# Optimization experiments

Hardware: AMD Instinct MI355X
Metric: run time of the kernel (lower is better)

## Reference

```python
import jax, jax.numpy as jnp
import numpy as np
import math

STATE_DIM = 512
NUM_GROUPS = 32
VMD_MODES = 8
PERM_DIM = 4
MAX_PATTERNS = math.factorial(PERM_DIM)  # 24


def setup_inputs() -> dict:
    key = jax.random.key(0)
    B, T = 16, 4096
    hidden_states = jax.random.normal(key, (B, T, STATE_DIM), dtype=jnp.float32)
    return {"hidden_states": hidden_states}


def _vmd_decomposition(signals):
    # signals: [B, G, T] -> modes [B, G, K, T]
    B, G, T = signals.shape
    K = VMD_MODES
    fft_signal = jnp.fft.fft(signals, axis=2)
    freqs = jnp.fft.fftfreq(T).astype(jnp.float32)
    bandwidth = 1.0 / K
    center_freqs = jnp.linspace(-0.5, 0.5, K, dtype=jnp.float32)
    dist = jnp.abs(freqs[None, :] - center_freqs[:, None])          # [K, T]
    filters = jnp.exp(-0.5 * (dist / bandwidth) ** 2)
    filtered = fft_signal[:, :, None, :] * filters[None, None, :, :]
    return jnp.fft.ifft(filtered, axis=3).real.astype(jnp.float32)


def _pattern_ids(windows):
    # windows: [B, G, K, N, m] -> Lehmer-code pattern ids [B, G, K, N]
    m = windows.shape[-1]
    si = jnp.argsort(windows, axis=-1)
    fact = [math.factorial(j) for j in range(m)]
    pid = jnp.zeros(windows.shape[:-1], dtype=jnp.int32)
    for i in range(m - 1):
        smaller = (si[..., i:i + 1] > si[..., i + 1:]).sum(axis=-1).astype(jnp.int32)
        pid = pid + smaller * fact[m - 1 - i]
    return pid


def _tmptm(modes):
    # modes: [B, G, K, T] -> normalized transition histogram [B, G, MP^2]
    B, G, K, T = modes.shape
    m, MP = PERM_DIM, MAX_PATTERNS
    N = T - m + 1
    # unfold(3, m, 1): [B, G, K, N, m]
    windows = jnp.stack([modes[..., i:i + N] for i in range(m)], axis=-1)
    pid = _pattern_ids(windows)                       # [B, G, K, N]
    lin = pid[..., :-1] * MP + pid[..., 1:]           # [B, G, K, N-1]
    # fused scatter-add histogram over (K, N-1) per (B, G) -- replaces one_hot+sum
    offset = jnp.arange(B * G, dtype=jnp.int32).reshape(B, G, 1, 1) * (MP * MP)
    flat = (lin + offset).reshape(-1)
    counts = jnp.zeros(B * G * MP * MP, dtype=jnp.float32).at[flat].add(1.0)
    tmptm = counts.reshape(B, G, MP * MP)
    row_sums = jnp.maximum(tmptm.sum(axis=2, keepdims=True), 1.0)
    return tmptm / row_sums


def _fmptm(modes):
    # modes: [B, G, K, T] -> upper-triangular energy correlations [B, G, K*(K-1)/2]
    B, G, K, T = modes.shape
    energies = modes ** 2
    mean_e = energies.mean(axis=3, keepdims=True)
    std_e = jnp.maximum(energies.std(axis=3, keepdims=True, ddof=1), 1e-8)  # torch std is unbiased
    ne = (energies - mean_e) / std_e
    corr = jnp.einsum('bgkt,bglt->bgkl', ne, ne) / T
    iu, ju = jnp.triu_indices(K, k=1)
    return corr[:, :, iu, ju]


def reference(hidden_states):
    B, T, D = hidden_states.shape
    G = NUM_GROUPS
    spg = D // G
    hs = hidden_states.astype(jnp.float32)
    hs = hs.transpose(0, 2, 1).reshape(B, G, spg, T)
    group_pooled = hs.mean(axis=2)                    # [B, G, T]
    modes = _vmd_decomposition(group_pooled)          # [B, G, K, T]
    tmptm = _tmptm(modes)
    fmptm = _fmptm(modes)
    return tmptm, fmptm
```

## Files before the change

### kernel.cpp

```cpp
#include <hip/hip_runtime.h>
#include <hip/hip_fp16.h>

#define TT   4096
#define NTH  512
#define SK(e) ((e) + (((e) >> 4) << 1))
#define ARR  4608
#define SM_FLOATS (4*ARR + 1152 + 44)
#define SM_BYTES  (SM_FLOATS * 4)

__device__ __forceinline__ float centerF(int k){
    return (float)(-0.5 + (double)k * (1.0/7.0));
}
__device__ __forceinline__ float freq_of(int m){
    return (float)((m < TT/2) ? m : (m - TT)) * (1.0f/(float)TT);
}
__device__ __forceinline__ float filtv(float f, float ck){
    float d = (f - ck) * 8.0f;
    return __expf(-0.5f * d * d);
}
__device__ __forceinline__ float Gval(int m, float ck){
    int mm = (TT - m) & (TT - 1);
    return (filtv(freq_of(m), ck) + filtv(freq_of(mm), ck)) * (0.5f/(float)TT);
}

struct C4 { float r0,i0,r1,i1,r2,i2,r3,i3; };

template<int SGN>
__device__ __forceinline__ void bf4(float c0r,float c0i,float c1r,float c1i,
                                    float c2r,float c2i,float c3r,float c3i,
                                    float ur,float ui, C4& o){
    float u2r = ur*ur - ui*ui, u2i = 2.f*ur*ui;
    float u3r = u2r*ur - u2i*ui, u3i = u2r*ui + u2i*ur;
    if (SGN < 0){ ui = -ui; u2i = -u2i; u3i = -u3i; }
    float ar = u2r*c2r - u2i*c2i, ai = u2r*c2i + u2i*c2r;
    float br = ur*c1r  - ui*c1i,  bi = ur*c1i  + ui*c1r;
    float er = u3r*c3r - u3i*c3i, ei = u3r*c3i + u3i*c3r;
    float s0r = c0r+ar, s0i = c0i+ai, s1r = c0r-ar, s1i = c0i-ai;
    float s2r = br+er,  s2i = bi+ei,  s3r = br-er,  s3i = bi-ei;
    o.r0 = s0r+s2r; o.i0 = s0i+s2i;
    o.r2 = s0r-s2r; o.i2 = s0i-s2i;
    if (SGN > 0){ o.r1 = s1r-s3i; o.i1 = s1i+s3r; o.r3 = s1r+s3i; o.i3 = s1i-s3r; }
    else        { o.r1 = s1r+s3i; o.i1 = s1i-s3r; o.r3 = s1r-s3i; o.i3 = s1i+s3r; }
}

template<int SGN>
__device__ __forceinline__ void stageLDS(const float* __restrict__ sr, const float* __restrict__ si,
                                         float* __restrict__ dr, float* __restrict__ di,
                                         int Ns, float uAr,float uAi,float uBr,float uBi, int tid){
#pragma unroll
    for (int h = 0; h < 2; ++h){
        int j = tid + h*512;
        float ur = h ? uBr : uAr, ui = h ? uBi : uAi;
        int kk = j & (Ns-1);
        int base = ((j & ~(Ns-1)) << 2) | kk;
        C4 o;
        bf4<SGN>(sr[SK(j)],si[SK(j)], sr[SK(j+1024)],si[SK(j+1024)],
                 sr[SK(j+2048)],si[SK(j+2048)], sr[SK(j+3072)],si[SK(j+3072)], ur,ui,o);
        dr[SK(base)]       = o.r0;  di[SK(base)]       = o.i0;
        dr[SK(base+Ns)]    = o.r1;  di[SK(base+Ns)]    = o.i1;
        dr[SK(base+2*Ns)]  = o.r2;  di[SK(base+2*Ns)]  = o.i2;
        dr[SK(base+3*Ns)]  = o.r3;  di[SK(base+3*Ns)]  = o.i3;
    }
}

__device__ __forceinline__ int wt_of(int r){ return r==0 ? 6 : (r==1 ? 2 : (r==2 ? 1 : 0)); }

__device__ __forceinline__ int pattern_id(float v0, float v1, float v2, float v3){
    int c01 = (v0 <= v1), c02 = (v0 <= v2), c03 = (v0 <= v3);
    int c12 = (v1 <= v2), c13 = (v1 <= v3), c23 = (v2 <= v3);
    int r1 = c01 + (1-c12) + (1-c13);
    int r2 = c02 + c12 + (1-c23);
    int r3 = c03 + c13 + c23;
    int g1 = 1 - c01;
    int g2 = (1-c02) + (1-c12);
    int g3 = (1-c03) + (1-c13) + (1-c23);
    return wt_of(r1)*g1 + wt_of(r2)*g2 + wt_of(r3)*g3;
}

__device__ __forceinline__ int DIDX(int k, int l){
    return 8 + k*8 + l - (k*(k+1))/2;
}

__device__ __forceinline__ void reduce_to(float v, float* res, int idx, int tid){
#pragma unroll
    for (int off = 32; off; off >>= 1) v += __shfl_xor(v, off);
    if ((tid & 63) == 0) atomicAdd(&res[idx], v);
}

template<int P>
__device__ __forceinline__ void process_pair(int tid,
        float* Ar, float* Ai, float* Br, float* Bi,
        unsigned* hist, float* res,
        const float (&xr)[8], const float (&xi)[8],
        __half2 (&est)[6][4],
        float t4r,float t4i,float t16r,float t16i,float t64r,float t64i,
        float t256r,float t256i,float tAr,float tAi,float tBr,float tBi){
    const float ck0 = centerF(2*P), ck1 = centerF(2*P+1);

#pragma unroll
    for (int h = 0; h < 2; ++h){
        int j = tid + h*512;
        float cr[4], ci[4];
#pragma unroll
        for (int q = 0; q < 4; ++q){
            int v = 2*q + h;
            int m = j + 1024*q;
            float g0 = Gval(m, ck0), g1 = Gval(m, ck1);
            cr[q] = xr[v]*g0 - xi[v]*g1;
            ci[q] = xi[v]*g0 + xr[v]*g1;
        }
        C4 o; bf4<1>(cr[0],ci[0],cr[1],ci[1],cr[2],ci[2],cr[3],ci[3], 1.f,0.f, o);
        int base = 4*j;
        Ar[SK(base)]   = o.r0;  Ai[SK(base)]   = o.i0;
        Ar[SK(base+1)] = o.r1;  Ai[SK(base+1)] = o.i1;
        Ar[SK(base+2)] = o.r2;  Ai[SK(base+2)] = o.i2;
        Ar[SK(base+3)] = o.r3;  Ai[SK(base+3)] = o.i3;
    }
    __syncthreads();
    stageLDS<1>(Ar,Ai,Br,Bi,    4, t4r,t4i,t4r,t4i, tid);       __syncthreads();
    stageLDS<1>(Br,Bi,Ar,Ai,   16, t16r,t16i,t16r,t16i, tid);   __syncthreads();
    stageLDS<1>(Ar,Ai,Br,Bi,   64, t64r,t64i,t64r,t64i, tid);   __syncthreads();
    stageLDS<1>(Br,Bi,Ar,Ai,  256, t256r,t256i,t256r,t256i, tid); __syncthreads();
    stageLDS<1>(Ar,Ai,Br,Bi, 1024, tAr,tAi,tBr,tBi, tid);       __syncthreads();

    int* pidR = (int*)Ar;
    int* pidI = (int*)Ai;

    float aS0=0.f, aS1=0.f, aD00=0.f, aD11=0.f, aD01=0.f;
    float aX[(P > 0) ? 4*P : 1];
#pragma unroll
    for (int i = 0; i < ((P>0)?4*P:1); ++i) aX[i] = 0.f;

    float carry0 = 0.f, carry1 = 0.f;
#pragma unroll
    for (int u = 0; u < 8; ++u){
        int t  = tid + u*NTH;
        int t1 = (t+1 < TT) ? t+1 : TT-1;
        int t2 = (t+2 < TT) ? t+2 : TT-1;
        int t3 = (t+3 < TT) ? t+3 : TT-1;
        float b0 = Br[SK(t)], b1 = Br[SK(t1)], b2 = Br[SK(t2)], b3 = Br[SK(t3)];
        float i0 = Bi[SK(t)], i1 = Bi[SK(t1)], i2 = Bi[SK(t2)], i3 = Bi[SK(t3)];
        float e0 = b0*b0, e1 = i0*i0;
        aS0 += e0; aS1 += e1;
        aD00 += e0*e0; aD11 += e1*e1; aD01 += e0*e1;
#pragma unroll
        for (int l = 0; l < 2*P; ++l){
            float el = (u & 1) ? __high2float(est[l][u>>1]) : __low2float(est[l][u>>1]);
            aX[2*l]   += el * e0;
            aX[2*l+1] += el * e1;
        }
        if constexpr (P < 3){
            if ((u & 1) == 0){ carry0 = e0; carry1 = e1; }
            else {
                est[2*P][u>>1]   = __floats2half2_rn(carry0, e0);
                est[2*P+1][u>>1] = __floats2half2_rn(carry1, e1);
            }
        }
        if (t <= TT-4){
            pidR[t] = pattern_id(b0,b1,b2,b3);
            pidI[t] = pattern_id(i0,i1,i2,i3);
        }
    }
    __syncthreads();

    {
        unsigned* h = hist + 576*((tid>>6) & 1);
        int curR = -1, curI = -1; unsigned cR = 0, cI = 0;
#pragma unroll
        for (int u = 0; u < 8; ++u){
            int t = tid + u*NTH;
            if (t <= TT-5){
                int lr = pidR[t]*24 + pidR[t+1];
                if (lr == curR) cR++;
                else { if (cR) atomicAdd(&h[curR], cR); curR = lr; cR = 1; }
                int li = pidI[t]*24 + pidI[t+1];
                if (li == curI) cI++;
                else { if (cI) atomicAdd(&h[curI], cI); curI = li; cI = 1; }
            }
        }
        if (cR) atomicAdd(&h[curR], cR);
        if (cI) atomicAdd(&h[curI], cI);
    }
    __syncthreads();

    const int k0 = 2*P, k1 = 2*P+1;
    reduce_to(aS0,  res, k0, tid);
    reduce_to(aS1,  res, k1, tid);
    reduce_to(aD00, res, DIDX(k0,k0), tid);
    reduce_to(aD11, res, DIDX(k1,k1), tid);
    reduce_to(aD01, res, DIDX(k0,k1), tid);
#pragma unroll
    for (int l = 0; l < 2*P; ++l){
        reduce_to(aX[2*l],   res, DIDX(l,k0), tid);
        reduce_to(aX[2*l+1], res, DIDX(l,k1), tid);
    }
}

template<bool DIRECT>
__global__ __launch_bounds__(NTH)
__attribute__((amdgpu_waves_per_eu(4,4)))
void fused_kernel(const float* __restrict__ hs, const float* __restrict__ pooled,
                  float* __restrict__ out){
    extern __shared__ float smem[];
    float* Ar = smem;
    float* Ai = smem + ARR;
    float* Br = smem + 2*ARR;
    float* Bi = smem + 3*ARR;
    unsigned* hist = (unsigned*)(smem + 4*ARR);
    float* res = smem + 4*ARR + 1152;

    const int tid = threadIdx.x;
    const int bg = blockIdx.x, b = bg >> 5, g = bg & 31;

    for (int i = tid; i < 1152; i += NTH) hist[i] = 0u;
    if (tid < 44) res[tid] = 0.f;

    const float PI_F = 3.14159265358979323846f;
    float t4r,t4i,t16r,t16i,t64r,t64i,t256r,t256i,tAr,tAi,tBr,tBi;
    { float s,c;
      __sincosf(PI_F*(float)(tid &   3)/   8.f, &s,&c); t4r=c;   t4i=s;
      __sincosf(PI_F*(float)(tid &  15)/  32.f, &s,&c); t16r=c;  t16i=s;
      __sincosf(PI_F*(float)(tid &  63)/ 128.f, &s,&c); t64r=c;  t64i=s;
      __sincosf(PI_F*(float)(tid & 255)/ 512.f, &s,&c); t256r=c; t256i=s;
      __sincosf(PI_F*(float)tid        /2048.f, &s,&c); tAr=c;   tAi=s;
      __sincosf(PI_F*(float)(tid+512)  /2048.f, &s,&c); tBr=c;   tBi=s;
    }

    if (DIRECT){
        const float* base = hs + ((size_t)b * TT) * 512 + g * 16;
#pragma unroll
        for (int u = 0; u < 8; ++u){
            int t = tid + u*NTH;
            const float4* p = (const float4*)(base + (size_t)t * 512);
            float4 a = p[0], bb = p[1], cc = p[2], dd = p[3];
            float s = a.x+a.y+a.z+a.w + bb.x+bb.y+bb.z+bb.w
                    + cc.x+cc.y+cc.z+cc.w + dd.x+dd.y+dd.z+dd.w;
            Ar[SK(t)] = s * (1.0f/16.0f);
            Ai[SK(t)] = 0.f;
        }
    } else {
        const float* pp = pooled + (size_t)bg * TT;
#pragma unroll
        for (int u = 0; u < 8; ++u){
            int t = tid + u*NTH;
            Ar[SK(t)] = pp[t];
            Ai[SK(t)] = 0.f;
        }
    }
    __syncthreads();

    stageLDS<-1>(Ar,Ai,Br,Bi,   1, 1.f,0.f,1.f,0.f, tid);        __syncthreads();
    stageLDS<-1>(Br,Bi,Ar,Ai,   4, t4r,t4i,t4r,t4i, tid);        __syncthreads();
    stageLDS<-1>(Ar,Ai,Br,Bi,  16, t16r,t16i,t16r,t16i, tid);    __syncthreads();
    stageLDS<-1>(Br,Bi,Ar,Ai,  64, t64r,t64i,t64r,t64i, tid);    __syncthreads();
    stageLDS<-1>(Ar,Ai,Br,Bi, 256, t256r,t256i,t256r,t256i, tid);__syncthreads();

    float xr[8], xi[8];
    {
        C4 o;
        bf4<-1>(Br[SK(tid)],Bi[SK(tid)], Br[SK(tid+1024)],Bi[SK(tid+1024)],
                Br[SK(tid+2048)],Bi[SK(tid+2048)], Br[SK(tid+3072)],Bi[SK(tid+3072)],
                tAr,tAi,o);
        xr[0]=o.r0; xi[0]=o.i0; xr[2]=o.r1; xi[2]=o.i1;
        xr[4]=o.r2; xi[4]=o.i2; xr[6]=o.r3; xi[6]=o.i3;
        bf4<-1>(Br[SK(tid+512)],Bi[SK(tid+512)], Br[SK(tid+1536)],Bi[SK(tid+1536)],
                Br[SK(tid+2560)],Bi[SK(tid+2560)], Br[SK(tid+3584)],Bi[SK(tid+3584)],
                tBr,tBi,o);
        xr[1]=o.r0; xi[1]=o.i0; xr[3]=o.r1; xi[3]=o.i1;
        xr[5]=o.r2; xi[5]=o.i2; xr[7]=o.r3; xi[7]=o.i3;
    }

    __half2 est[6][4];
    process_pair<0>(tid,Ar,Ai,Br,Bi,hist,res,xr,xi,est,t4r,t4i,t16r,t16i,t64r,t64i,t256r,t256i,tAr,tAi,tBr,tBi);
    process_pair<1>(tid,Ar,Ai,Br,Bi,hist,res,xr,xi,est,t4r,t4i,t16r,t16i,t64r,t64i,t256r,t256i,tAr,tAi,tBr,tBi);
    process_pair<2>(tid,Ar,Ai,Br,Bi,hist,res,xr,xi,est,t4r,t4i,t16r,t16i,t64r,t64i,t256r,t256i,tAr,tAi,tBr,tBi);
    process_pair<3>(tid,Ar,Ai,Br,Bi,hist,res,xr,xi,est,t4r,t4i,t16r,t16i,t64r,t64i,t256r,t256i,tAr,tAi,tBr,tBi);

    __syncthreads();

    float* tm = out + (size_t)bg * 576;
    for (int i = tid; i < 576; i += NTH)
        tm[i] = (float)(hist[i] + hist[i+576]) * (1.0f/32736.0f);

    if (tid < 28){
        int q = tid, k = 0, cnt = 7, rem = q;
        while (rem >= cnt){ rem -= cnt; k++; cnt--; }
        int l = k + 1 + rem;
        float Sk = res[k], Sl = res[l];
        float Dkl = res[DIDX(k,l)], Dkk = res[DIDX(k,k)], Dll = res[DIDX(l,l)];
        float cov = Dkl - Sk*Sl*(1.0f/4096.0f);
        float vk = (Dkk - Sk*Sk*(1.0f/4096.0f)) * (1.0f/4095.0f);
        float vl = (Dll - Sl*Sl*(1.0f/4096.0f)) * (1.0f/4095.0f);
        float sk = fmaxf(sqrtf(fmaxf(vk, 0.f)), 1e-8f);
        float sl = fmaxf(sqrtf(fmaxf(vl, 0.f)), 1e-8f);
        out[294912 + (size_t)bg*28 + q] = cov * (1.0f/4096.0f) / (sk*sl);
    }
}

__global__ __launch_bounds__(256)
void pool_kernel(const float* __restrict__ hs, float* __restrict__ pooled){
    __shared__ float tile[32][65];
    int blk = blockIdx.x;
    int b   = blk >> 6;
    int t0  = (blk & 63) << 6;
    int tid = threadIdx.x;
    int lane = tid & 63, wid = tid >> 6;
#pragma unroll
    for (int i = 0; i < 16; ++i){
        int tl = wid + i*4;
        int t  = t0 + tl;
        const float4* p = (const float4*)(hs + ((size_t)b * TT + t) * 512);
        float4 a = p[lane];
        float4 c = p[lane + 64];
        float pa = a.x+a.y+a.z+a.w;
        float pc = c.x+c.y+c.z+c.w;
        pa += __shfl_xor(pa, 1); pa += __shfl_xor(pa, 2);
        pc += __shfl_xor(pc, 1); pc += __shfl_xor(pc, 2);
        if ((lane & 3) == 0){
            int gq = lane >> 2;
            tile[gq][tl]      = pa * (1.0f/16.0f);
            tile[gq + 16][tl] = pc * (1.0f/16.0f);
        }
    }
    __syncthreads();
    for (int idx = tid; idx < 2048; idx += 256){
        int g = idx >> 6, tt = idx & 63;
        pooled[((size_t)b * 32 + g) * TT + t0 + tt] = tile[g][tt];
    }
}

extern "C" void kernel_launch(void* const* d_in, const int* in_sizes, int n_in,
                              void* d_out, int out_size, void* d_ws, size_t ws_size,
                              hipStream_t stream){
    const float* hs = (const float*)d_in[0];
    float* out = (float*)d_out;
    const size_t poolBytes = (size_t)512 * TT * sizeof(float);

    if (d_ws && ws_size >= poolBytes){
        float* pooled = (float*)d_ws;
        pool_kernel<<<1024, 256, 0, stream>>>(hs, pooled);
        hipFuncSetAttribute((const void*)fused_kernel<false>,
                            hipFuncAttributeMaxDynamicSharedMemorySize, SM_BYTES);
        fused_kernel<false><<<512, NTH, SM_BYTES, stream>>>(hs, pooled, out);
    } else {
        hipFuncSetAttribute((const void*)fused_kernel<true>,
                            hipFuncAttributeMaxDynamicSharedMemorySize, SM_BYTES);
        fused_kernel<true><<<512, NTH, SM_BYTES, stream>>>(hs, nullptr, out);
    }
}
```

Measured before the change: 320.5 us.

## Switch 4096-point LDS FFT from radix-4 to radix-8 stages

```diff
diff --git a/kernel.cpp b/kernel.cpp
--- a/kernel.cpp
+++ b/kernel.cpp
@@ -3,8 +3,8 @@
 
 #define TT   4096
 #define NTH  512
-#define SK(e) ((e) + (((e) >> 4) << 1))
-#define ARR  4608
+#define SK(e) ((e) + ((e) >> 5))
+#define ARR  4224
 #define SM_FLOATS (4*ARR + 1152 + 44)
 #define SM_BYTES  (SM_FLOATS * 4)
 
@@ -23,43 +23,75 @@
     return (filtv(freq_of(m), ck) + filtv(freq_of(mm), ck)) * (0.5f/(float)TT);
 }
 
-struct C4 { float r0,i0,r1,i1,r2,i2,r3,i3; };
-
 template<int SGN>
-__device__ __forceinline__ void bf4(float c0r,float c0i,float c1r,float c1i,
-                                    float c2r,float c2i,float c3r,float c3i,
-                                    float ur,float ui, C4& o){
-    float u2r = ur*ur - ui*ui, u2i = 2.f*ur*ui;
-    float u3r = u2r*ur - u2i*ui, u3i = u2r*ui + u2i*ur;
-    if (SGN < 0){ ui = -ui; u2i = -u2i; u3i = -u3i; }
-    float ar = u2r*c2r - u2i*c2i, ai = u2r*c2i + u2i*c2r;
-    float br = ur*c1r  - ui*c1i,  bi = ur*c1i  + ui*c1r;
-    float er = u3r*c3r - u3i*c3i, ei = u3r*c3i + u3i*c3r;
-    float s0r = c0r+ar, s0i = c0i+ai, s1r = c0r-ar, s1i = c0i-ai;
-    float s2r = br+er,  s2i = bi+ei,  s3r = br-er,  s3i = bi-ei;
-    o.r0 = s0r+s2r; o.i0 = s0i+s2i;
-    o.r2 = s0r-s2r; o.i2 = s0i-s2i;
-    if (SGN > 0){ o.r1 = s1r-s3i; o.i1 = s1i+s3r; o.r3 = s1r+s3i; o.i3 = s1i-s3r; }
-    else        { o.r1 = s1r+s3i; o.i1 = s1i-s3r; o.r3 = s1r-s3i; o.i3 = s1i+s3r; }
-}
-
-template<int SGN>
-__device__ __forceinline__ void stageLDS(const float* __restrict__ sr, const float* __restrict__ si,
-                                         float* __restrict__ dr, float* __restrict__ di,
-                                         int Ns, float uAr,float uAi,float uBr,float uBi, int tid){
-#pragma unroll
-    for (int h = 0; h < 2; ++h){
-        int j = tid + h*512;
-        float ur = h ? uBr : uAr, ui = h ? uBi : uAi;
-        int kk = j & (Ns-1);
-        int base = ((j & ~(Ns-1)) << 2) | kk;
-        C4 o;
-        bf4<SGN>(sr[SK(j)],si[SK(j)], sr[SK(j+1024)],si[SK(j+1024)],
-                 sr[SK(j+2048)],si[SK(j+2048)], sr[SK(j+3072)],si[SK(j+3072)], ur,ui,o);
-        dr[SK(base)]       = o.r0;  di[SK(base)]       = o.i0;
-        dr[SK(base+Ns)]    = o.r1;  di[SK(base+Ns)]    = o.i1;
-        dr[SK(base+2*Ns)]  = o.r2;  di[SK(base+2*Ns)]  = o.i2;
-        dr[SK(base+3*Ns)]  = o.r3;  di[SK(base+3*Ns)]  = o.i3;
+__device__ __forceinline__ void bf8(float (&xr)[8], float (&xi)[8]){
+    const float C = 0.7071067811865476f;
+    float tr[4], ti[4], ur[4], ui[4];
+#pragma unroll
+    for (int p = 0; p < 4; ++p){
+        tr[p] = xr[p] + xr[p+4]; ti[p] = xi[p] + xi[p+4];
+        ur[p] = xr[p] - xr[p+4]; ui[p] = xi[p] - xi[p+4];
+    }
+    float vr[4], vi[4];
+    vr[0] = ur[0]; vi[0] = ui[0];
+    if (SGN > 0){
+        vr[1] =  C*(ur[1] - ui[1]); vi[1] =  C*(ur[1] + ui[1]);
+        vr[2] = -ui[2];             vi[2] =  ur[2];
+        vr[3] = -C*(ur[3] + ui[3]); vi[3] =  C*(ur[3] - ui[3]);
+    } else {
+        vr[1] =  C*(ur[1] + ui[1]); vi[1] =  C*(ui[1] - ur[1]);
+        vr[2] =  ui[2];             vi[2] = -ur[2];
+        vr[3] =  C*(ui[3] - ur[3]); vi[3] = -C*(ur[3] + ui[3]);
+    }
+    {
+        float s0r=tr[0]+tr[2], s0i=ti[0]+ti[2], s1r=tr[0]-tr[2], s1i=ti[0]-ti[2];
+        float s2r=tr[1]+tr[3], s2i=ti[1]+ti[3], s3r=tr[1]-tr[3], s3i=ti[1]-ti[3];
+        xr[0]=s0r+s2r; xi[0]=s0i+s2i;
+        xr[4]=s0r-s2r; xi[4]=s0i-s2i;
+        if (SGN > 0){ xr[2]=s1r-s3i; xi[2]=s1i+s3r; xr[6]=s1r+s3i; xi[6]=s1i-s3r; }
+        else        { xr[2]=s1r+s3i; xi[2]=s1i-s3r; xr[6]=s1r-s3i; xi[6]=s1i+s3r; }
+    }
+    {
+        float s0r=vr[0]+vr[2], s0i=vi[0]+vi[2], s1r=vr[0]-vr[2], s1i=vi[0]-vi[2];
+        float s2r=vr[1]+vr[3], s2i=vi[1]+vi[3], s3r=vr[1]-vr[3], s3i=vi[1]-vi[3];
+        xr[1]=s0r+s2r; xi[1]=s0i+s2i;
+        xr[5]=s0r-s2r; xi[5]=s0i-s2i;
+        if (SGN > 0){ xr[3]=s1r-s3i; xi[3]=s1i+s3r; xr[7]=s1r+s3i; xi[7]=s1i-s3r; }
+        else        { xr[3]=s1r+s3i; xi[3]=s1i-s3r; xr[7]=s1r-s3i; xi[7]=s1i+s3r; }
+    }
+}
+
+__device__ __forceinline__ void twid8(float (&xr)[8], float (&xi)[8], float wr, float wi){
+    float pr = wr, pi = wi;
+#pragma unroll
+    for (int q = 1; q < 8; ++q){
+        float ar = xr[q], ai = xi[q];
+        xr[q] = ar*pr - ai*pi;
+        xi[q] = ar*pi + ai*pr;
+        float nr = pr*wr - pi*wi;
+        float ni = pr*wi + pi*wr;
+        pr = nr; pi = ni;
+    }
+}
+
+template<int SGN, int NS>
+__device__ __forceinline__ void stage8(const float* __restrict__ sr, const float* __restrict__ si,
+                                       float* __restrict__ dr, float* __restrict__ di,
+                                       float wr, float wi, int tid){
+    float xr[8], xi[8];
+#pragma unroll
+    for (int q = 0; q < 8; ++q){
+        xr[q] = sr[SK(tid + 512*q)];
+        xi[q] = si[SK(tid + 512*q)];
+    }
+    if (NS > 1) twid8(xr, xi, wr, wi);
+    bf8<SGN>(xr, xi);
+    int kk = tid & (NS-1);
+    int base = ((tid & ~(NS-1)) << 3) | kk;
+#pragma unroll
+    for (int m = 0; m < 8; ++m){
+        dr[SK(base + m*NS)] = xr[m];
+        di[SK(base + m*NS)] = xi[m];
     }
 }
 
@@ -93,35 +125,45 @@
         unsigned* hist, float* res,
         const float (&xr)[8], const float (&xi)[8],
         __half2 (&est)[6][4],
-        float t4r,float t4i,float t16r,float t16i,float t64r,float t64i,
-        float t256r,float t256i,float tAr,float tAi,float tBr,float tBi){
+        float w8r,float w8i,float w64r,float w64i,float w512r,float w512i){
     const float ck0 = centerF(2*P), ck1 = centerF(2*P+1);
 
-#pragma unroll
-    for (int h = 0; h < 2; ++h){
-        int j = tid + h*512;
-        float cr[4], ci[4];
-#pragma unroll
-        for (int q = 0; q < 4; ++q){
-            int v = 2*q + h;
-            int m = j + 1024*q;
+    {
+        float cr[8], ci[8];
+#pragma unroll
+        for (int q = 0; q < 8; ++q){
+            int m = tid + 512*q;
             float g0 = Gval(m, ck0), g1 = Gval(m, ck1);
-            cr[q] = xr[v]*g0 - xi[v]*g1;
-            ci[q] = xi[v]*g0 + xr[v]*g1;
-        }
-        C4 o; bf4<1>(cr[0],ci[0],cr[1],ci[1],cr[2],ci[2],cr[3],ci[3], 1.f,0.f, o);
-        int base = 4*j;
-        Ar[SK(base)]   = o.r0;  Ai[SK(base)]   = o.i0;
-        Ar[SK(base+1)] = o.r1;  Ai[SK(base+1)] = o.i1;
-        Ar[SK(base+2)] = o.r2;  Ai[SK(base+2)] = o.i2;
-        Ar[SK(base+3)] = o.r3;  Ai[SK(base+3)] = o.i3;
-    }
-    __syncthreads();
-    stageLDS<1>(Ar,Ai,Br,Bi,    4, t4r,t4i,t4r,t4i, tid);       __syncthreads();
-    stageLDS<1>(Br,Bi,Ar,Ai,   16, t16r,t16i,t16r,t16i, tid);   __syncthreads();
-    stageLDS<1>(Ar,Ai,Br,Bi,   64, t64r,t64i,t64r,t64i, tid);   __syncthreads();
-    stageLDS<1>(Br,Bi,Ar,Ai,  256, t256r,t256i,t256r,t256i, tid); __syncthreads();
-    stageLDS<1>(Ar,Ai,Br,Bi, 1024, tAr,tAi,tBr,tBi, tid);       __syncthreads();
+            cr[q] = xr[q]*g0 - xi[q]*g1;
+            ci[q] = xi[q]*g0 + xr[q]*g1;
+        }
+        bf8<1>(cr, ci);
+        int base = 8*tid;
+#pragma unroll
+        for (int m = 0; m < 8; ++m){
+            Ar[SK(base+m)] = cr[m];
+            Ai[SK(base+m)] = ci[m];
+        }
+    }
+    __syncthreads();
+    stage8<1,8>(Ar,Ai,Br,Bi, w8r,w8i, tid);    __syncthreads();
+    stage8<1,64>(Br,Bi,Ar,Ai, w64r,w64i, tid); __syncthreads();
+
+    float yr[8], yi[8];
+#pragma unroll
+    for (int q = 0; q < 8; ++q){
+        yr[q] = Ar[SK(tid + 512*q)];
+        yi[q] = Ai[SK(tid + 512*q)];
+    }
+    twid8(yr, yi, w512r, w512i);
+    bf8<1>(yr, yi);
+#pragma unroll
+    for (int m = 0; m < 8; ++m){
+        int t = tid + 512*m;
+        Br[SK(t)] = yr[m];
+        Bi[SK(t)] = yi[m];
+    }
+    __syncthreads();
 
     int* pidR = (int*)Ar;
     int* pidI = (int*)Ai;
@@ -134,12 +176,13 @@
     float carry0 = 0.f, carry1 = 0.f;
 #pragma unroll
     for (int u = 0; u < 8; ++u){
-        int t  = tid + u*NTH;
+        int t  = tid + 512*u;
         int t1 = (t+1 < TT) ? t+1 : TT-1;
         int t2 = (t+2 < TT) ? t+2 : TT-1;
         int t3 = (t+3 < TT) ? t+3 : TT-1;
-        float b0 = Br[SK(t)], b1 = Br[SK(t1)], b2 = Br[SK(t2)], b3 = Br[SK(t3)];
-        float i0 = Bi[SK(t)], i1 = Bi[SK(t1)], i2 = Bi[SK(t2)], i3 = Bi[SK(t3)];
+        float b0 = yr[u],       i0 = yi[u];
+        float b1 = Br[SK(t1)],  b2 = Br[SK(t2)], b3 = Br[SK(t3)];
+        float j1 = Bi[SK(t1)],  j2 = Bi[SK(t2)], j3 = Bi[SK(t3)];
         float e0 = b0*b0, e1 = i0*i0;
         aS0 += e0; aS1 += e1;
         aD00 += e0*e0; aD11 += e1*e1; aD01 += e0*e1;
@@ -158,7 +201,7 @@
         }
         if (t <= TT-4){
             pidR[t] = pattern_id(b0,b1,b2,b3);
-            pidI[t] = pattern_id(i0,i1,i2,i3);
+            pidI[t] = pattern_id(i0,j1,j2,j3);
         }
     }
     __syncthreads();
@@ -168,7 +211,7 @@
         int curR = -1, curI = -1; unsigned cR = 0, cI = 0;
 #pragma unroll
         for (int u = 0; u < 8; ++u){
-            int t = tid + u*NTH;
+            int t = tid + 512*u;
             if (t <= TT-5){
                 int lr = pidR[t]*24 + pidR[t+1];
                 if (lr == curR) cR++;
@@ -181,7 +224,6 @@
         if (cR) atomicAdd(&h[curR], cR);
         if (cI) atomicAdd(&h[curI], cI);
     }
-    __syncthreads();
 
     const int k0 = 2*P, k1 = 2*P+1;
     reduce_to(aS0,  res, k0, tid);
@@ -194,11 +236,11 @@
         reduce_to(aX[2*l],   res, DIDX(l,k0), tid);
         reduce_to(aX[2*l+1], res, DIDX(l,k1), tid);
     }
+    __syncthreads();
 }
 
 template<bool DIRECT>
-__global__ __launch_bounds__(NTH)
-__attribute__((amdgpu_waves_per_eu(4,4)))
+__global__ __launch_bounds__(NTH, 1)
 void fused_kernel(const float* __restrict__ hs, const float* __restrict__ pooled,
                   float* __restrict__ out){
     extern __shared__ float smem[];
@@ -216,14 +258,11 @@
     if (tid < 44) res[tid] = 0.f;
 
     const float PI_F = 3.14159265358979323846f;
-    float t4r,t4i,t16r,t16i,t64r,t64i,t256r,t256i,tAr,tAi,tBr,tBi;
+    float w8r,w8i,w64r,w64i,w512r,w512i;
     { float s,c;
-      __sincosf(PI_F*(float)(tid &   3)/   8.f, &s,&c); t4r=c;   t4i=s;
-      __sincosf(PI_F*(float)(tid &  15)/  32.f, &s,&c); t16r=c;  t16i=s;
-      __sincosf(PI_F*(float)(tid &  63)/ 128.f, &s,&c); t64r=c;  t64i=s;
-      __sincosf(PI_F*(float)(tid & 255)/ 512.f, &s,&c); t256r=c; t256i=s;
-      __sincosf(PI_F*(float)tid        /2048.f, &s,&c); tAr=c;   tAi=s;
-      __sincosf(PI_F*(float)(tid+512)  /2048.f, &s,&c); tBr=c;   tBi=s;
+      __sincosf(PI_F*(float)(tid &  7)/  32.f, &s,&c); w8r=c;   w8i=s;
+      __sincosf(PI_F*(float)(tid & 63)/ 256.f, &s,&c); w64r=c;  w64i=s;
+      __sincosf(PI_F*(float)tid       /2048.f, &s,&c); w512r=c; w512i=s;
     }
 
     if (DIRECT){
@@ -249,34 +288,27 @@
     }
     __syncthreads();
 
-    stageLDS<-1>(Ar,Ai,Br,Bi,   1, 1.f,0.f,1.f,0.f, tid);        __syncthreads();
-    stageLDS<-1>(Br,Bi,Ar,Ai,   4, t4r,t4i,t4r,t4i, tid);        __syncthreads();
-    stageLDS<-1>(Ar,Ai,Br,Bi,  16, t16r,t16i,t16r,t16i, tid);    __syncthreads();
-    stageLDS<-1>(Br,Bi,Ar,Ai,  64, t64r,t64i,t64r,t64i, tid);    __syncthreads();
-    stageLDS<-1>(Ar,Ai,Br,Bi, 256, t256r,t256i,t256r,t256i, tid);__syncthreads();
+    stage8<-1,1>(Ar,Ai,Br,Bi, 1.f,0.f, tid);        __syncthreads();
+    stage8<-1,8>(Br,Bi,Ar,Ai, w8r,-w8i, tid);       __syncthreads();
+    stage8<-1,64>(Ar,Ai,Br,Bi, w64r,-w64i, tid);    __syncthreads();
 
     float xr[8], xi[8];
     {
-        C4 o;
-        bf4<-1>(Br[SK(tid)],Bi[SK(tid)], Br[SK(tid+1024)],Bi[SK(tid+1024)],
-                Br[SK(tid+2048)],Bi[SK(tid+2048)], Br[SK(tid+3072)],Bi[SK(tid+3072)],
-                tAr,tAi,o);
-        xr[0]=o.r0; xi[0]=o.i0; xr[2]=o.r1; xi[2]=o.i1;
-        xr[4]=o.r2; xi[4]=o.i2; xr[6]=o.r3; xi[6]=o.i3;
-        bf4<-1>(Br[SK(tid+512)],Bi[SK(tid+512)], Br[SK(tid+1536)],Bi[SK(tid+1536)],
-                Br[SK(tid+2560)],Bi[SK(tid+2560)], Br[SK(tid+3584)],Bi[SK(tid+3584)],
-                tBr,tBi,o);
-        xr[1]=o.r0; xi[1]=o.i0; xr[3]=o.r1; xi[3]=o.i1;
-        xr[5]=o.r2; xi[5]=o.i2; xr[7]=o.r3; xi[7]=o.i3;
+#pragma unroll
+        for (int q = 0; q < 8; ++q){
+            xr[q] = Br[SK(tid + 512*q)];
+            xi[q] = Bi[SK(tid + 512*q)];
+        }
+        twid8(xr, xi, w512r, -w512i);
+        bf8<-1>(xr, xi);
     }
 
     __half2 est[6][4];
-    process_pair<0>(tid,Ar,Ai,Br,Bi,hist,res,xr,xi,est,t4r,t4i,t16r,t16i,t64r,t64i,t256r,t256i,tAr,tAi,tBr,tBi);
-    process_pair<1>(tid,Ar,Ai,Br,Bi,hist,res,xr,xi,est,t4r,t4i,t16r,t16i,t64r,t64i,t256r,t256i,tAr,tAi,tBr,tBi);
-    process_pair<2>(tid,Ar,Ai,Br,Bi,hist,res,xr,xi,est,t4r,t4i,t16r,t16i,t64r,t64i,t256r,t256i,tAr,tAi,tBr,tBi);
-    process_pair<3>(tid,Ar,Ai,Br,Bi,hist,res,xr,xi,est,t4r,t4i,t16r,t16i,t64r,t64i,t256r,t256i,tAr,tAi,tBr,tBi);
-
-    __syncthreads();
+    process_pair<0>(tid,Ar,Ai,Br,Bi,hist,res,xr,xi,est,w8r,w8i,w64r,w64i,w512r,w512i);
+    process_pair<1>(tid,Ar,Ai,Br,Bi,hist,res,xr,xi,est,w8r,w8i,w64r,w64i,w512r,w512i);
+    process_pair<2>(tid,Ar,Ai,Br,Bi,hist,res,xr,xi,est,w8r,w8i,w64r,w64i,w512r,w512i);
+    process_pair<3>(tid,Ar,Ai,Br,Bi,hist,res,xr,xi,est,w8r,w8i,w64r,w64i,w512r,w512i);
+
 
     float* tm = out + (size_t)bg * 576;
     for (int i = tid; i < 576; i += NTH)
```

After: 291.3 us. -9.1%, faster.
